# Optimization experiments

Measured on AMD Instinct MI355X. Metric: run time of the kernel, lower is better.

## Reference

```python
import jax, jax.numpy as jnp
import numpy as np

BS, L, D, N, K = 2048, 100, 256, 16, 32
M_CONST = 2
NEG = -1e9


def setup_inputs() -> dict:
    key = jax.random.key(0)
    ks = jax.random.split(key, 6)
    hist = jax.random.normal(ks[0], (BS, L, D), dtype=jnp.float32)
    hist_mask = jnp.ones((BS, L), dtype=jnp.float32)  # passed but unused by PolyAttention (faithful)
    cand = jax.random.normal(ks[1], (BS, N, D), dtype=jnp.float32)
    num_interests = jax.random.randint(ks[2], (BS,), 1, K + 1, dtype=jnp.int32)
    cat_counts = jax.random.randint(ks[3], (BS,), 1, 21, dtype=jnp.int32)
    W_poly = jax.random.normal(ks[4], (D, D), dtype=jnp.float32) * (1.0 / np.sqrt(D))
    context_codes = jax.random.normal(ks[5], (K, D), dtype=jnp.float32) * (1.0 / np.sqrt(D))
    return {
        "history_news_representations": hist,
        "history_mask": hist_mask,
        "candidate_news_representations": cand,
        "num_extracted_interests": num_interests,
        "unique_category_counts": cat_counts,
        "W_poly": W_poly,
        "context_codes": context_codes,
    }


def _forward(hist, hist_mask, cand, num_interests, cat_counts, W_poly, context_codes):
    # --- PolyAttention ---
    proj = jnp.tanh(jnp.einsum("bld,ed->ble", hist, W_poly))        # [bs, L, ccd]
    weights = jnp.einsum("ble,ke->bkl", proj, context_codes)         # [bs, K, L]
    cc_mask = jnp.arange(K)[None, :] < num_interests[:, None]        # [bs, K]
    weights = jnp.where(cc_mask[:, :, None], weights, NEG)
    weights = jax.nn.softmax(weights, axis=2)
    weights = jnp.nan_to_num(weights, nan=0.0, posinf=0.0, neginf=0.0)
    interests = jnp.einsum("bkl,bld->bkd", weights, hist)            # [bs, K, d]

    # --- InterestCandidateAttention over all N candidates at once ---
    aw = jnp.einsum("bkd,bnd->bnk", interests, cand)                 # [bs, N, K]
    dyn_K = jnp.ceil(jnp.log2(M_CONST * cat_counts.astype(jnp.float32))).astype(jnp.int32)
    dyn_K = jnp.clip(dyn_K, 1, K)                                    # [bs]
    # rank of each entry in descending order along K
    order = jnp.argsort(-aw, axis=-1)
    rank = jnp.argsort(order, axis=-1)                               # [bs, N, K]
    topk_mask = (rank < dyn_K[:, None, None]).astype(aw.dtype)
    masked = aw * topk_mask
    user = jnp.einsum("bnk,bkd->bnd", masked, interests)             # [bs, N, d]
    return user


def reference(history_news_representations, history_mask, candidate_news_representations,
              num_extracted_interests, unique_category_counts, W_poly, context_codes):
    return _forward(history_news_representations, history_mask, candidate_news_representations,
                    num_extracted_interests, unique_category_counts, W_poly, context_codes)
```

## Files before the change

kernel.cpp:

```cpp
#include <hip/hip_runtime.h>
#include <math.h>

#define NEGV (-1e9f)

typedef _Float16 half8 __attribute__((ext_vector_type(8)));
typedef float f32x4 __attribute__((ext_vector_type(4)));


__device__ inline float tanh_fast(float x) {
    float t = __expf(2.0f * x);
    float r = __builtin_amdgcn_rcpf(t + 1.0f);
    return fmaf(-2.0f, r, 1.0f);
}

__device__ inline void split8(const float4 a, const float4 b, half8& h, half8& m) {
    const float* pa = (const float*)&a;
    const float* pb = (const float*)&b;
    #pragma unroll
    for (int q = 0; q < 4; ++q) {
        float x = pa[q];
        _Float16 hi = (_Float16)x;
        h[q] = hi; m[q] = (_Float16)(x - (float)hi);
    }
    #pragma unroll
    for (int q = 0; q < 4; ++q) {
        float x = pb[q];
        _Float16 hi = (_Float16)x;
        h[4+q] = hi; m[4+q] = (_Float16)(x - (float)hi);
    }
}

__device__ inline void gload_lds16(const void* g, void* lds) {
    __builtin_amdgcn_global_load_lds(
        (const __attribute__((address_space(1))) unsigned int*)g,
        (__attribute__((address_space(3))) unsigned int*)lds, 16, 0, 0);
}

__global__ __launch_bounds__(256)
void k_prep(const float* __restrict__ W, half8* __restrict__ Wf)
{
    int slot = blockIdx.x * 256 + threadIdx.x;
    int kt = slot >> 10;
    int ct = (slot >> 6) & 15;
    int lane = slot & 63;
    int e = ct * 16 + (lane & 15);
    int g = lane >> 4;
    const float* src = &W[(size_t)e * 256 + kt * 32 + g * 8];
    float4 a = *(const float4*)src;
    float4 b = *(const float4*)(src + 4);
    half8 h, m;
    split8(a, b, h, m);
    Wf[((kt * 2 + 0) * 16 + ct) * 64 + lane] = h;
    Wf[((kt * 2 + 1) * 16 + ct) * 64 + lane] = m;
}

__global__ __launch_bounds__(256, 2)
void k_proj_logits(const float* __restrict__ hist, const half8* __restrict__ Wf,
                   const float* __restrict__ cc, float* __restrict__ logits)
{
    __shared__ __align__(16) char smem[49152];
    _Float16* Af = (_Float16*)smem;
    _Float16* Bf = (_Float16*)(smem + 16384);
    float (*Pj)[68] = (float(*)[68])smem;

    const int tid  = threadIdx.x;
    const int lane = tid & 63;
    const int w    = tid >> 6;
    const int wr   = w >> 1, wc = w & 1;
    const int g    = lane >> 4;
    const int r    = lane & 15;
    const size_t rowBase = (size_t)blockIdx.x * 128;

    f32x4 acc[4][8];
    #pragma unroll
    for (int i = 0; i < 4; ++i)
        #pragma unroll
        for (int j = 0; j < 8; ++j) acc[i][j] = (f32x4)(0.0f);

    const float* aSrc0 = &hist[(rowBase + (size_t)(w    ) * 16 + r) * 256 + g * 8];
    const float* aSrc1 = &hist[(rowBase + (size_t)(w + 4) * 16 + r) * 256 + g * 8];

    float4 a00 = *(const float4*)aSrc0;
    float4 a01 = *(const float4*)(aSrc0 + 4);
    float4 a10 = *(const float4*)aSrc1;
    float4 a11 = *(const float4*)(aSrc1 + 4);

    for (int kt = 0; kt < 8; ++kt) {
        __syncthreads();
        {
            const char* wsrc = (const char*)Wf + (size_t)kt * 32768 + tid * 16;
            char* ldst = smem + 16384 + (tid & 192) * 16;
            #pragma unroll
            for (int i = 0; i < 8; ++i)
                gload_lds16(wsrc + i * 4096, ldst + i * 4096);
        }
        {
            half8 h, m;
            split8(a00, a01, h, m);
            int u = w * 64 + lane;
            *(half8*)&Af[u * 8] = h;
            *(half8*)&Af[(512 + u) * 8] = m;
            split8(a10, a11, h, m);
            u = (w + 4) * 64 + lane;
            *(half8*)&Af[u * 8] = h;
            *(half8*)&Af[(512 + u) * 8] = m;
        }
        if (kt < 7) {
            int off = (kt + 1) * 32;
            a00 = *(const float4*)(aSrc0 + off);
            a01 = *(const float4*)(aSrc0 + off + 4);
            a10 = *(const float4*)(aSrc1 + off);
            a11 = *(const float4*)(aSrc1 + off + 4);
        }
        __syncthreads();

        half8 Ah[4], Am[4];
        #pragma unroll
        for (int rt = 0; rt < 4; ++rt) {
            int u = (wr * 4 + rt) * 64 + lane;
            Ah[rt] = *(half8*)&Af[u * 8];
            Am[rt] = *(half8*)&Af[(512 + u) * 8];
        }
        #pragma unroll
        for (int ct = 0; ct < 8; ++ct) {
            int ctg = wc * 8 + ct;
            half8 Bh = *(half8*)&Bf[(ctg * 64 + lane) * 8];
            half8 Bm = *(half8*)&Bf[((1024 + ctg * 64 + lane)) * 8];
            #pragma unroll
            for (int rt = 0; rt < 4; ++rt) {
                acc[rt][ct] = __builtin_amdgcn_mfma_f32_16x16x32_f16(Ah[rt], Bh, acc[rt][ct], 0, 0, 0);
                acc[rt][ct] = __builtin_amdgcn_mfma_f32_16x16x32_f16(Ah[rt], Bm, acc[rt][ct], 0, 0, 0);
                acc[rt][ct] = __builtin_amdgcn_mfma_f32_16x16x32_f16(Am[rt], Bh, acc[rt][ct], 0, 0, 0);
            }
        }
    }

    f32x4 acc2[2][2];
    #pragma unroll
    for (int i = 0; i < 2; ++i)
        #pragma unroll
        for (int j = 0; j < 2; ++j) acc2[i][j] = (f32x4)(0.0f);

    #pragma unroll
    for (int ec = 0; ec < 4; ++ec) {
        __syncthreads();
        if (wc == (ec >> 1)) {
            #pragma unroll
            for (int rt = 0; rt < 4; ++rt) {
                #pragma unroll
                for (int c4i = 0; c4i < 4; ++c4i) {
                    int ctm = (ec & 1) * 4 + c4i;
                    f32x4 t = acc[rt][ctm];
                    int el = c4i * 16 + r;
                    int rb = 64 * wr + rt * 16 + g * 4;
                    #pragma unroll
                    for (int i = 0; i < 4; ++i)
                        Pj[rb + i][el] = tanh_fast(t[i]);
                }
            }
        }
        __syncthreads();
        #pragma unroll
        for (int ks = 0; ks < 2; ++ks) {
            half8 Ah2[2], Am2[2];
            #pragma unroll
            for (int rt2 = 0; rt2 < 2; ++rt2) {
                const float* src = &Pj[32 * w + rt2 * 16 + r][ks * 32 + g * 8];
                float4 p0 = *(const float4*)src;
                float4 p1 = *(const float4*)(src + 4);
                split8(p0, p1, Ah2[rt2], Am2[rt2]);
            }
            #pragma unroll
            for (int ct = 0; ct < 2; ++ct) {
                const float* csrc = &cc[(size_t)(ct * 16 + r) * 256 + 64 * ec + ks * 32 + g * 8];
                float4 q0 = *(const float4*)csrc;
                float4 q1 = *(const float4*)(csrc + 4);
                half8 Bh, Bm;
                split8(q0, q1, Bh, Bm);
                #pragma unroll
                for (int rt2 = 0; rt2 < 2; ++rt2) {
                    acc2[rt2][ct] = __builtin_amdgcn_mfma_f32_16x16x32_f16(Ah2[rt2], Bh, acc2[rt2][ct], 0, 0, 0);
                    acc2[rt2][ct] = __builtin_amdgcn_mfma_f32_16x16x32_f16(Ah2[rt2], Bm, acc2[rt2][ct], 0, 0, 0);
                    acc2[rt2][ct] = __builtin_amdgcn_mfma_f32_16x16x32_f16(Am2[rt2], Bh, acc2[rt2][ct], 0, 0, 0);
                }
            }
        }
    }
    #pragma unroll
    for (int rt2 = 0; rt2 < 2; ++rt2)
        #pragma unroll
        for (int ct = 0; ct < 2; ++ct)
            #pragma unroll
            for (int i = 0; i < 4; ++i) {
                size_t grow = rowBase + 32 * w + rt2 * 16 + g * 4 + i;
                logits[grow * 32 + ct * 16 + r] = acc2[rt2][ct][i];
            }
}

__global__ __launch_bounds__(256, 3)
void k_attn(const float* __restrict__ hist, const float* __restrict__ cand,
            const int* __restrict__ numi, const int* __restrict__ catc,
            const float* __restrict__ logits, float* __restrict__ out)
{
    __shared__ float wT[100][36];
    __shared__ float ib[32][260];
    __shared__ float aws[16][36];
    __shared__ float maw[16][36];

    const int tid = threadIdx.x;
    const int b = blockIdx.x;
    const int num = numi[b];

    for (int idx = tid; idx < 3200; idx += 256) {
        int l = idx >> 5;
        int k = idx & 31;
        wT[l][k] = logits[(size_t)b * 3200 + idx];
    }
    __syncthreads();

    {
        const int k = tid >> 3;
        const int lg = tid & 7;
        const bool valid = k < num;
        float vals[13];
        float m = -INFINITY;
        #pragma unroll
        for (int i = 0; i < 13; ++i) {
            int l = lg + 8 * i;
            if (l < 100) {
                float v = valid ? wT[l][k] : NEGV;
                vals[i] = v;
                m = fmaxf(m, v);
            }
        }
        #pragma unroll
        for (int off = 1; off < 8; off <<= 1)
            m = fmaxf(m, __shfl_xor(m, off, 8));
        float s = 0.0f;
        #pragma unroll
        for (int i = 0; i < 13; ++i) {
            int l = lg + 8 * i;
            if (l < 100) {
                float e = expf(vals[i] - m);
                s += e;
                wT[l][k] = e;
            }
        }
        #pragma unroll
        for (int off = 1; off < 8; off <<= 1)
            s += __shfl_xor(s, off, 8);
        float inv = 1.0f / s;
        #pragma unroll
        for (int i = 0; i < 13; ++i) {
            int l = lg + 8 * i;
            if (l < 100) wT[l][k] *= inv;
        }
    }
    __syncthreads();

    {
        float acc[32];
        #pragma unroll
        for (int k = 0; k < 32; ++k) acc[k] = 0.0f;

        #pragma unroll
        for (int s = 0; s < 4; ++s) {
            int idx = tid + s * 256;
            int lp = idx >> 6;
            int c4 = (idx & 63) * 4;
            *(float4*)&ib[lp][c4] = *(const float4*)&hist[((size_t)b * 100 + lp) * 256 + c4];
        }
        __syncthreads();

        for (int c = 0; c < 7; ++c) {
            float4 pre[4];
            if (c < 6) {
                #pragma unroll
                for (int s = 0; s < 4; ++s) {
                    int idx = tid + s * 256;
                    int lp = idx >> 6;
                    int c4 = (idx & 63) * 4;
                    int l = 16 * (c + 1) + lp;
                    pre[s] = (l < 100) ? *(const float4*)&hist[((size_t)b * 100 + l) * 256 + c4]
                                       : float4{0.f, 0.f, 0.f, 0.f};
                }
            }
            int rows = (c == 6) ? 4 : 16;
            const int rb = (c & 1) * 16;
            #pragma unroll 4
            for (int lp = 0; lp < rows; ++lp) {
                float h = ib[rb + lp][tid];
                const float4* wrow = (const float4*)wT[16 * c + lp];
                #pragma unroll
                for (int kq = 0; kq < 8; ++kq) {
                    float4 w4 = wrow[kq];
                    acc[4 * kq + 0] = fmaf(w4.x, h, acc[4 * kq + 0]);
                    acc[4 * kq + 1] = fmaf(w4.y, h, acc[4 * kq + 1]);
                    acc[4 * kq + 2] = fmaf(w4.z, h, acc[4 * kq + 2]);
                    acc[4 * kq + 3] = fmaf(w4.w, h, acc[4 * kq + 3]);
                }
            }
            if (c < 6) {
                const int wb = ((c + 1) & 1) * 16;
                #pragma unroll
                for (int s = 0; s < 4; ++s) {
                    int idx = tid + s * 256;
                    int lp = idx >> 6;
                    int c4 = (idx & 63) * 4;
                    *(float4*)&ib[wb + lp][c4] = pre[s];
                }
            }
            __syncthreads();
        }
        #pragma unroll
        for (int k = 0; k < 32; ++k) ib[k][tid] = acc[k];
    }
    __syncthreads();

    {
        const int n = tid & 15;
        const int kq = tid >> 4;
        const float4* cg = (const float4*)&cand[((size_t)b * 16 + n) * 256];
        const float4* i0 = (const float4*)&ib[kq][0];
        const float4* i1 = (const float4*)&ib[kq + 16][0];
        float s0 = 0.0f, s1 = 0.0f;
        for (int q = 0; q < 64; ++q) {
            float4 cv = cg[q];
            float4 a0 = i0[q];
            float4 a1 = i1[q];
            s0 += a0.x * cv.x + a0.y * cv.y + a0.z * cv.z + a0.w * cv.w;
            s1 += a1.x * cv.x + a1.y * cv.y + a1.z * cv.z + a1.w * cv.w;
        }
        aws[n][kq] = s0;
        aws[n][kq + 16] = s1;
    }
    __syncthreads();

    {
        int c = catc[b];
        int dynK = 32 - __clz(2 * c - 1);
        const int k = tid & 31;
        const int n1 = tid >> 5;
        #pragma unroll
        for (int h = 0; h < 2; ++h) {
            int n = n1 + 8 * h;
            float a = aws[n][k];
            int cnt = 0;
            #pragma unroll
            for (int j = 0; j < 32; ++j) {
                float aj = aws[n][j];
                cnt += (aj > a) || (aj == a && j < k);
            }
            maw[n][k] = (cnt < dynK) ? a : 0.0f;
        }
    }
    __syncthreads();

    {
        const int dd = tid & 63;
        const int ng = tid >> 6;
        float4 acc4[4];
        #pragma unroll
        for (int nn = 0; nn < 4; ++nn) { acc4[nn].x = acc4[nn].y = acc4[nn].z = acc4[nn].w = 0.0f; }
        for (int k = 0; k < 32; ++k) {
            float4 iv = *(const float4*)&ib[k][4 * dd];
            #pragma unroll
            for (int nn = 0; nn < 4; ++nn) {
                float m = maw[4 * ng + nn][k];
                acc4[nn].x = fmaf(m, iv.x, acc4[nn].x);
                acc4[nn].y = fmaf(m, iv.y, acc4[nn].y);
                acc4[nn].z = fmaf(m, iv.z, acc4[nn].z);
                acc4[nn].w = fmaf(m, iv.w, acc4[nn].w);
            }
        }
        #pragma unroll
        for (int nn = 0; nn < 4; ++nn) {
            *(float4*)&out[((size_t)b * 16 + 4 * ng + nn) * 256 + 4 * dd] = acc4[nn];
        }
    }
}

extern "C" void kernel_launch(void* const* d_in, const int* in_sizes, int n_in,
                              void* d_out, int out_size, void* d_ws, size_t ws_size,
                              hipStream_t stream) {
    const float* hist = (const float*)d_in[0];
    const float* cand = (const float*)d_in[2];
    const int*   numi = (const int*)d_in[3];
    const int*   catc = (const int*)d_in[4];
    const float* W    = (const float*)d_in[5];
    const float* cc   = (const float*)d_in[6];
    float* out = (float*)d_out;
    float* logits = (float*)d_ws;
    const size_t LOG_BYTES = 26214400;
    const size_t WF_BYTES = 262144;
    half8* Wf = (ws_size >= LOG_BYTES + WF_BYTES)
                ? (half8*)((char*)d_ws + LOG_BYTES)
                : (half8*)d_out;

    k_prep<<<32, 256, 0, stream>>>(W, Wf);
    k_proj_logits<<<1600, 256, 0, stream>>>(hist, Wf, cc, logits);
    k_attn<<<2048, 256, 0, stream>>>(hist, cand, numi, catc, logits, out);
}
```

Before: 257.0 us.

## Drop LDS staging in projection GEMM, precompute context-code fragments, stream hist in attention

```diff
diff --git a/kernel.cpp b/kernel.cpp
--- a/kernel.cpp
+++ b/kernel.cpp
@@ -30,38 +30,46 @@
     }
 }
 
-__device__ inline void gload_lds16(const void* g, void* lds) {
-    __builtin_amdgcn_global_load_lds(
-        (const __attribute__((address_space(1))) unsigned int*)g,
-        (__attribute__((address_space(3))) unsigned int*)lds, 16, 0, 0);
-}
-
 __global__ __launch_bounds__(256)
-void k_prep(const float* __restrict__ W, half8* __restrict__ Wf)
+void k_prep(const float* __restrict__ W, const float* __restrict__ cc,
+            half8* __restrict__ Wf, half8* __restrict__ Cf)
 {
     int slot = blockIdx.x * 256 + threadIdx.x;
-    int kt = slot >> 10;
-    int ct = (slot >> 6) & 15;
-    int lane = slot & 63;
-    int e = ct * 16 + (lane & 15);
-    int g = lane >> 4;
-    const float* src = &W[(size_t)e * 256 + kt * 32 + g * 8];
-    float4 a = *(const float4*)src;
-    float4 b = *(const float4*)(src + 4);
-    half8 h, m;
-    split8(a, b, h, m);
-    Wf[((kt * 2 + 0) * 16 + ct) * 64 + lane] = h;
-    Wf[((kt * 2 + 1) * 16 + ct) * 64 + lane] = m;
+    if (slot < 8192) {
+        int kt = slot >> 10;
+        int ct = (slot >> 6) & 15;
+        int lane = slot & 63;
+        int e = ct * 16 + (lane & 15);
+        int g = lane >> 4;
+        const float* src = &W[(size_t)e * 256 + kt * 32 + g * 8];
+        float4 a = *(const float4*)src;
+        float4 b = *(const float4*)(src + 4);
+        half8 h, m;
+        split8(a, b, h, m);
+        Wf[((kt * 2 + 0) * 16 + ct) * 64 + lane] = h;
+        Wf[((kt * 2 + 1) * 16 + ct) * 64 + lane] = m;
+    } else if (slot < 9216) {
+        int s = slot - 8192;
+        int lane = s & 63;
+        int ct = (s >> 6) & 1;
+        int et = s >> 7;
+        int k2 = ct * 16 + (lane & 15);
+        int g = lane >> 4;
+        const float* src = &cc[(size_t)k2 * 256 + et * 32 + g * 8];
+        float4 a = *(const float4*)src;
+        float4 b = *(const float4*)(src + 4);
+        half8 h, m;
+        split8(a, b, h, m);
+        Cf[((et * 2 + 0) * 2 + ct) * 64 + lane] = h;
+        Cf[((et * 2 + 1) * 2 + ct) * 64 + lane] = m;
+    }
 }
 
 __global__ __launch_bounds__(256, 2)
 void k_proj_logits(const float* __restrict__ hist, const half8* __restrict__ Wf,
-                   const float* __restrict__ cc, float* __restrict__ logits)
+                   const half8* __restrict__ Cf, float* __restrict__ logits)
 {
-    __shared__ __align__(16) char smem[49152];
-    _Float16* Af = (_Float16*)smem;
-    _Float16* Bf = (_Float16*)(smem + 16384);
-    float (*Pj)[68] = (float(*)[68])smem;
+    __shared__ float Pj[128][68];
 
     const int tid  = threadIdx.x;
     const int lane = tid & 63;
@@ -77,55 +85,35 @@
         #pragma unroll
         for (int j = 0; j < 8; ++j) acc[i][j] = (f32x4)(0.0f);
 
-    const float* aSrc0 = &hist[(rowBase + (size_t)(w    ) * 16 + r) * 256 + g * 8];
-    const float* aSrc1 = &hist[(rowBase + (size_t)(w + 4) * 16 + r) * 256 + g * 8];
-
-    float4 a00 = *(const float4*)aSrc0;
-    float4 a01 = *(const float4*)(aSrc0 + 4);
-    float4 a10 = *(const float4*)aSrc1;
-    float4 a11 = *(const float4*)(aSrc1 + 4);
-
+    const float* aPtr = &hist[(rowBase + (size_t)wr * 64 + r) * 256 + g * 8];
+
+    float4 a0[4], a1[4];
+    #pragma unroll
+    for (int rt = 0; rt < 4; ++rt) {
+        const float* s = aPtr + rt * (16 * 256);
+        a0[rt] = *(const float4*)s;
+        a1[rt] = *(const float4*)(s + 4);
+    }
+
+    #pragma unroll
     for (int kt = 0; kt < 8; ++kt) {
-        __syncthreads();
-        {
-            const char* wsrc = (const char*)Wf + (size_t)kt * 32768 + tid * 16;
-            char* ldst = smem + 16384 + (tid & 192) * 16;
-            #pragma unroll
-            for (int i = 0; i < 8; ++i)
-                gload_lds16(wsrc + i * 4096, ldst + i * 4096);
-        }
-        {
-            half8 h, m;
-            split8(a00, a01, h, m);
-            int u = w * 64 + lane;
-            *(half8*)&Af[u * 8] = h;
-            *(half8*)&Af[(512 + u) * 8] = m;
-            split8(a10, a11, h, m);
-            u = (w + 4) * 64 + lane;
-            *(half8*)&Af[u * 8] = h;
-            *(half8*)&Af[(512 + u) * 8] = m;
-        }
+        half8 Ah[4], Am[4];
+        #pragma unroll
+        for (int rt = 0; rt < 4; ++rt)
+            split8(a0[rt], a1[rt], Ah[rt], Am[rt]);
         if (kt < 7) {
-            int off = (kt + 1) * 32;
-            a00 = *(const float4*)(aSrc0 + off);
-            a01 = *(const float4*)(aSrc0 + off + 4);
-            a10 = *(const float4*)(aSrc1 + off);
-            a11 = *(const float4*)(aSrc1 + off + 4);
-        }
-        __syncthreads();
-
-        half8 Ah[4], Am[4];
-        #pragma unroll
-        for (int rt = 0; rt < 4; ++rt) {
-            int u = (wr * 4 + rt) * 64 + lane;
-            Ah[rt] = *(half8*)&Af[u * 8];
-            Am[rt] = *(half8*)&Af[(512 + u) * 8];
+            #pragma unroll
+            for (int rt = 0; rt < 4; ++rt) {
+                const float* s = aPtr + rt * (16 * 256) + (kt + 1) * 32;
+                a0[rt] = *(const float4*)s;
+                a1[rt] = *(const float4*)(s + 4);
+            }
         }
         #pragma unroll
         for (int ct = 0; ct < 8; ++ct) {
             int ctg = wc * 8 + ct;
-            half8 Bh = *(half8*)&Bf[(ctg * 64 + lane) * 8];
-            half8 Bm = *(half8*)&Bf[((1024 + ctg * 64 + lane)) * 8];
+            half8 Bh = Wf[(size_t)((kt * 2 + 0) * 16 + ctg) * 64 + lane];
+            half8 Bm = Wf[(size_t)((kt * 2 + 1) * 16 + ctg) * 64 + lane];
             #pragma unroll
             for (int rt = 0; rt < 4; ++rt) {
                 acc[rt][ct] = __builtin_amdgcn_mfma_f32_16x16x32_f16(Ah[rt], Bh, acc[rt][ct], 0, 0, 0);
@@ -170,13 +158,11 @@
                 float4 p1 = *(const float4*)(src + 4);
                 split8(p0, p1, Ah2[rt2], Am2[rt2]);
             }
+            int et = ec * 2 + ks;
             #pragma unroll
             for (int ct = 0; ct < 2; ++ct) {
-                const float* csrc = &cc[(size_t)(ct * 16 + r) * 256 + 64 * ec + ks * 32 + g * 8];
-                float4 q0 = *(const float4*)csrc;
-                float4 q1 = *(const float4*)(csrc + 4);
-                half8 Bh, Bm;
-                split8(q0, q1, Bh, Bm);
+                half8 Bh = Cf[((et * 2 + 0) * 2 + ct) * 64 + lane];
+                half8 Bm = Cf[((et * 2 + 1) * 2 + ct) * 64 + lane];
                 #pragma unroll
                 for (int rt2 = 0; rt2 < 2; ++rt2) {
                     acc2[rt2][ct] = __builtin_amdgcn_mfma_f32_16x16x32_f16(Ah2[rt2], Bh, acc2[rt2][ct], 0, 0, 0);
@@ -203,7 +189,7 @@
             const float* __restrict__ logits, float* __restrict__ out)
 {
     __shared__ float wT[100][36];
-    __shared__ float ib[32][260];
+    __shared__ float ints[32][260];
     __shared__ float aws[16][36];
     __shared__ float maw[16][36];
 
@@ -259,61 +245,29 @@
     __syncthreads();
 
     {
-        float acc[32];
-        #pragma unroll
-        for (int k = 0; k < 32; ++k) acc[k] = 0.0f;
-
-        #pragma unroll
-        for (int s = 0; s < 4; ++s) {
-            int idx = tid + s * 256;
-            int lp = idx >> 6;
-            int c4 = (idx & 63) * 4;
-            *(float4*)&ib[lp][c4] = *(const float4*)&hist[((size_t)b * 100 + lp) * 256 + c4];
-        }
-        __syncthreads();
-
-        for (int c = 0; c < 7; ++c) {
-            float4 pre[4];
-            if (c < 6) {
-                #pragma unroll
-                for (int s = 0; s < 4; ++s) {
-                    int idx = tid + s * 256;
-                    int lp = idx >> 6;
-                    int c4 = (idx & 63) * 4;
-                    int l = 16 * (c + 1) + lp;
-                    pre[s] = (l < 100) ? *(const float4*)&hist[((size_t)b * 100 + l) * 256 + c4]
-                                       : float4{0.f, 0.f, 0.f, 0.f};
-                }
-            }
-            int rows = (c == 6) ? 4 : 16;
-            const int rb = (c & 1) * 16;
-            #pragma unroll 4
-            for (int lp = 0; lp < rows; ++lp) {
-                float h = ib[rb + lp][tid];
-                const float4* wrow = (const float4*)wT[16 * c + lp];
-                #pragma unroll
-                for (int kq = 0; kq < 8; ++kq) {
-                    float4 w4 = wrow[kq];
-                    acc[4 * kq + 0] = fmaf(w4.x, h, acc[4 * kq + 0]);
-                    acc[4 * kq + 1] = fmaf(w4.y, h, acc[4 * kq + 1]);
-                    acc[4 * kq + 2] = fmaf(w4.z, h, acc[4 * kq + 2]);
-                    acc[4 * kq + 3] = fmaf(w4.w, h, acc[4 * kq + 3]);
-                }
-            }
-            if (c < 6) {
-                const int wb = ((c + 1) & 1) * 16;
-                #pragma unroll
-                for (int s = 0; s < 4; ++s) {
-                    int idx = tid + s * 256;
-                    int lp = idx >> 6;
-                    int c4 = (idx & 63) * 4;
-                    *(float4*)&ib[wb + lp][c4] = pre[s];
-                }
-            }
-            __syncthreads();
-        }
-        #pragma unroll
-        for (int k = 0; k < 32; ++k) ib[k][tid] = acc[k];
+        const int dq = tid & 63;
+        const int kh = tid >> 6;
+        float4 a4[8];
+        #pragma unroll
+        for (int kk = 0; kk < 8; ++kk) { a4[kk].x = a4[kk].y = a4[kk].z = a4[kk].w = 0.0f; }
+        const float4* hrow = (const float4*)&hist[(size_t)b * 25600] + dq;
+        #pragma unroll 4
+        for (int l = 0; l < 100; ++l) {
+            float4 hv = hrow[(size_t)l * 64];
+            float4 w0 = *(const float4*)&wT[l][8 * kh];
+            float4 w1 = *(const float4*)&wT[l][8 * kh + 4];
+            float wv[8] = {w0.x, w0.y, w0.z, w0.w, w1.x, w1.y, w1.z, w1.w};
+            #pragma unroll
+            for (int kk = 0; kk < 8; ++kk) {
+                a4[kk].x = fmaf(wv[kk], hv.x, a4[kk].x);
+                a4[kk].y = fmaf(wv[kk], hv.y, a4[kk].y);
+                a4[kk].z = fmaf(wv[kk], hv.z, a4[kk].z);
+                a4[kk].w = fmaf(wv[kk], hv.w, a4[kk].w);
+            }
+        }
+        #pragma unroll
+        for (int kk = 0; kk < 8; ++kk)
+            *(float4*)&ints[8 * kh + kk][4 * dq] = a4[kk];
     }
     __syncthreads();
 
@@ -321,15 +275,15 @@
         const int n = tid & 15;
         const int kq = tid >> 4;
         const float4* cg = (const float4*)&cand[((size_t)b * 16 + n) * 256];
-        const float4* i0 = (const float4*)&ib[kq][0];
-        const float4* i1 = (const float4*)&ib[kq + 16][0];
+        const float4* i0 = (const float4*)&ints[kq][0];
+        const float4* i1 = (const float4*)&ints[kq + 16][0];
         float s0 = 0.0f, s1 = 0.0f;
         for (int q = 0; q < 64; ++q) {
             float4 cv = cg[q];
-            float4 a0 = i0[q];
-            float4 a1 = i1[q];
-            s0 += a0.x * cv.x + a0.y * cv.y + a0.z * cv.z + a0.w * cv.w;
-            s1 += a1.x * cv.x + a1.y * cv.y + a1.z * cv.z + a1.w * cv.w;
+            float4 v0 = i0[q];
+            float4 v1 = i1[q];
+            s0 += v0.x * cv.x + v0.y * cv.y + v0.z * cv.z + v0.w * cv.w;
+            s1 += v1.x * cv.x + v1.y * cv.y + v1.z * cv.z + v1.w * cv.w;
         }
         aws[n][kq] = s0;
         aws[n][kq + 16] = s1;
@@ -363,7 +317,7 @@
         #pragma unroll
         for (int nn = 0; nn < 4; ++nn) { acc4[nn].x = acc4[nn].y = acc4[nn].z = acc4[nn].w = 0.0f; }
         for (int k = 0; k < 32; ++k) {
-            float4 iv = *(const float4*)&ib[k][4 * dd];
+            float4 iv = *(const float4*)&ints[k][4 * dd];
             #pragma unroll
             for (int nn = 0; nn < 4; ++nn) {
                 float m = maw[4 * ng + nn][k];
@@ -393,11 +347,14 @@
     float* logits = (float*)d_ws;
     const size_t LOG_BYTES = 26214400;
     const size_t WF_BYTES = 262144;
-    half8* Wf = (ws_size >= LOG_BYTES + WF_BYTES)
-                ? (half8*)((char*)d_ws + LOG_BYTES)
-                : (half8*)d_out;
-
-    k_prep<<<32, 256, 0, stream>>>(W, Wf);
-    k_proj_logits<<<1600, 256, 0, stream>>>(hist, Wf, cc, logits);
+    const size_t CF_BYTES = 32768;
+    char* fragBase = (ws_size >= LOG_BYTES + WF_BYTES + CF_BYTES)
+                     ? ((char*)d_ws + LOG_BYTES)
+                     : (char*)d_out;
+    half8* Wf = (half8*)fragBase;
+    half8* Cf = (half8*)(fragBase + WF_BYTES);
+
+    k_prep<<<36, 256, 0, stream>>>(W, cc, Wf, Cf);
+    k_proj_logits<<<1600, 256, 0, stream>>>(hist, Wf, Cf, logits);
     k_attn<<<2048, 256, 0, stream>>>(hist, cand, numi, catc, logits, out);
 }
```

Result: slower. 265.7 us (+3.4%).
